# Performance work log

Measured on AMD Instinct MI355X. Metric: run time of the kernel, lower is better.

The kernel has to match this reference:

```python
import jax, jax.numpy as jnp
import numpy as np

N_NODES = 50000
N_EDGES = 800000
D_IN = 128
D_HID = 128
D_OUT = 2


def setup_inputs() -> dict:
    key = jax.random.key(0)
    ks = jax.random.split(key, 8)
    x = jax.random.normal(ks[0], (N_NODES, D_IN), dtype=jnp.float32)
    edge_index = jax.random.randint(ks[1], (2, N_EDGES), 0, N_NODES, dtype=jnp.int64)
    s = 0.05
    W1_l = jax.random.normal(ks[2], (D_HID, D_IN), dtype=jnp.float32) * s
    W1_r = jax.random.normal(ks[3], (D_HID, D_IN), dtype=jnp.float32) * s
    b1 = jax.random.normal(ks[4], (D_HID,), dtype=jnp.float32) * s
    W2_l = jax.random.normal(ks[5], (D_OUT, D_HID), dtype=jnp.float32) * s
    W2_r = jax.random.normal(ks[6], (D_OUT, D_HID), dtype=jnp.float32) * s
    b2 = jax.random.normal(ks[7], (D_OUT,), dtype=jnp.float32) * s
    return {"x": x, "edge_index": edge_index, "W1_l": W1_l, "W1_r": W1_r,
            "b1": b1, "W2_l": W2_l, "W2_r": W2_r, "b2": b2}


def _sage_conv(x, src, dst, W_l, W_r, b):
    # mean-aggregate neighbor features: gather from src, scatter-sum to dst
    n = x.shape[0]
    msg = x[src]                                            # [E, d]
    agg = jax.ops.segment_sum(msg, dst, num_segments=n)      # [n, d]
    cnt = jax.ops.segment_sum(jnp.ones((src.shape[0],), x.dtype), dst,
                              num_segments=n)
    agg = agg / jnp.maximum(cnt, 1.0)[:, None]
    # lin_l(aggregated) + lin_r(self) + bias  (PyG SAGEConv with root_weight)
    return agg @ W_l.T + x @ W_r.T + b


def reference(x, edge_index, W1_l, W1_r, b1, W2_l, W2_r, b2):
    src, dst = edge_index[0], edge_index[1]
    h = _sage_conv(x, src, dst, W1_l, W1_r, b1)
    h = jax.nn.relu(h)
    out = _sage_conv(h, src, dst, W2_l, W2_r, b2)
    return out
```

## Files before the change

### kernel.cpp

```cpp
#include <hip/hip_runtime.h>

#define N_NODES 50000
#define N_EDGES 800000
#define CAP 48
#define NCHUNK 391

typedef __bf16 bf16_8 __attribute__((ext_vector_type(8)));
typedef float  f32_4  __attribute__((ext_vector_type(4)));
typedef unsigned short u16;
typedef unsigned char  u8;


__device__ __forceinline__ void f8cvt(int2 q, float f[8]) {
    f[0] = __builtin_amdgcn_cvt_f32_fp8(q.x, 0);
    f[1] = __builtin_amdgcn_cvt_f32_fp8(q.x, 1);
    f[2] = __builtin_amdgcn_cvt_f32_fp8(q.x, 2);
    f[3] = __builtin_amdgcn_cvt_f32_fp8(q.x, 3);
    f[4] = __builtin_amdgcn_cvt_f32_fp8(q.y, 0);
    f[5] = __builtin_amdgcn_cvt_f32_fp8(q.y, 1);
    f[6] = __builtin_amdgcn_cvt_f32_fp8(q.y, 2);
    f[7] = __builtin_amdgcn_cvt_f32_fp8(q.y, 3);
}

__global__ void prep_kernel(const float* __restrict__ W1l, const float* __restrict__ W1r,
                            __bf16* __restrict__ Wt, const float* __restrict__ x,
                            u8* __restrict__ xb8,
                            const int* __restrict__ src, const int* __restrict__ dst,
                            int* __restrict__ deg_p, u16* __restrict__ bins) {
    int b = blockIdx.x;
    if (b < 8 * NCHUNK) {
        const int chunk = b >> 3;
        const unsigned cls = b & 7;
        const int base = chunk * 2048;
        int t = base + (int)cls * 256 + threadIdx.x;
        if (t < 16 * N_NODES) {
            int node = t >> 4, c8 = t & 15;
            const f32_4* xp = (const f32_4*)(x + node * 128 + c8 * 8);
            f32_4 v0 = __builtin_nontemporal_load(xp);
            f32_4 v1 = __builtin_nontemporal_load(xp + 1);
            int lo = __builtin_amdgcn_cvt_pk_fp8_f32(v0[0], v0[1], 0, false);
            lo     = __builtin_amdgcn_cvt_pk_fp8_f32(v0[2], v0[3], lo, true);
            int hi = __builtin_amdgcn_cvt_pk_fp8_f32(v1[0], v1[1], 0, false);
            hi     = __builtin_amdgcn_cvt_pk_fp8_f32(v1[2], v1[3], hi, true);
            *(int2*)(xb8 + t * 8) = make_int2(lo, hi);
        }
        #pragma unroll
        for (int k = 0; k < 8; ++k) {
            int e = base + k * 256 + threadIdx.x;
            if (e < N_EDGES) {
                int d = dst[e];
                if (__umulhi((unsigned)d, 687195u) == cls) {
                    int s = src[e];
                    int pos = atomicAdd(&deg_p[d * 16], 1);
                    if (pos < CAP) bins[d * CAP + pos] = (u16)s;
                }
            }
        }
    } else {
        int t = (b - 8 * NCHUNK) * 256 + threadIdx.x;
        int n = t >> 8, k = t & 255;
        float v = (k < 128) ? W1l[n * 128 + k] : W1r[n * 128 + (k - 128)];
        Wt[t] = (__bf16)v;
    }
}

#define LDA 264
__global__ __launch_bounds__(256) void gather_gemm_kernel(
    const int* __restrict__ deg_p, const u16* __restrict__ bins,
    const float* __restrict__ x, const u8* __restrict__ xb8,
    const __bf16* __restrict__ Wt,
    const float* __restrict__ b1, const float* __restrict__ W2l,
    const float* __restrict__ W2r, float* __restrict__ y, float* __restrict__ z)
{
    __shared__ __bf16 As[16 * LDA];
    __shared__ float4 sp[4][16];

    const int i0 = blockIdx.x * 16;
    const int tid = threadIdx.x;
    const int row = tid >> 4, c8 = tid & 15;
    const int gi = i0 + row;

    {
        const f32_4* sxp = (const f32_4*)(x + gi * 128 + c8 * 8);
        f32_4 v0 = __builtin_nontemporal_load(sxp);
        f32_4 v1 = __builtin_nontemporal_load(sxp + 1);
        bf16_8 sv;
        sv[0] = (__bf16)v0[0]; sv[1] = (__bf16)v0[1]; sv[2] = (__bf16)v0[2]; sv[3] = (__bf16)v0[3];
        sv[4] = (__bf16)v1[0]; sv[5] = (__bf16)v1[1]; sv[6] = (__bf16)v1[2]; sv[7] = (__bf16)v1[3];
        *(bf16_8*)(&As[row * LDA + 128 + c8 * 8]) = sv;
    }

    {
        const u16* bp = bins + gi * CAP;
        int n = min(deg_p[gi * 16], CAP);
        float acc[8] = {};
        int j = 0;
        for (; j + 8 <= n; j += 8) {
            uint4 bq = *(const uint4*)(bp + j);
            int2 q0 = *(const int2*)(xb8 + (bq.x & 0xffff) * 128 + c8 * 8);
            int2 q1 = *(const int2*)(xb8 + (bq.x >> 16)    * 128 + c8 * 8);
            int2 q2 = *(const int2*)(xb8 + (bq.y & 0xffff) * 128 + c8 * 8);
            int2 q3 = *(const int2*)(xb8 + (bq.y >> 16)    * 128 + c8 * 8);
            int2 q4 = *(const int2*)(xb8 + (bq.z & 0xffff) * 128 + c8 * 8);
            int2 q5 = *(const int2*)(xb8 + (bq.z >> 16)    * 128 + c8 * 8);
            int2 q6 = *(const int2*)(xb8 + (bq.w & 0xffff) * 128 + c8 * 8);
            int2 q7 = *(const int2*)(xb8 + (bq.w >> 16)    * 128 + c8 * 8);
            float f0[8], f1[8], f2[8], f3[8], f4[8], f5[8], f6[8], f7[8];
            f8cvt(q0, f0); f8cvt(q1, f1); f8cvt(q2, f2); f8cvt(q3, f3);
            f8cvt(q4, f4); f8cvt(q5, f5); f8cvt(q6, f6); f8cvt(q7, f7);
            #pragma unroll
            for (int u = 0; u < 8; ++u)
                acc[u] += ((f0[u] + f1[u]) + (f2[u] + f3[u])) +
                          ((f4[u] + f5[u]) + (f6[u] + f7[u]));
        }
        if (j + 4 <= n) {
            uint2 bq = *(const uint2*)(bp + j);
            int2 q0 = *(const int2*)(xb8 + (bq.x & 0xffff) * 128 + c8 * 8);
            int2 q1 = *(const int2*)(xb8 + (bq.x >> 16)    * 128 + c8 * 8);
            int2 q2 = *(const int2*)(xb8 + (bq.y & 0xffff) * 128 + c8 * 8);
            int2 q3 = *(const int2*)(xb8 + (bq.y >> 16)    * 128 + c8 * 8);
            float f0[8], f1[8], f2[8], f3[8];
            f8cvt(q0, f0); f8cvt(q1, f1); f8cvt(q2, f2); f8cvt(q3, f3);
            #pragma unroll
            for (int u = 0; u < 8; ++u)
                acc[u] += (f0[u] + f1[u]) + (f2[u] + f3[u]);
            j += 4;
        }
        if (j + 2 <= n) {
            int i0e = bp[j], i1e = bp[j + 1];
            int2 q0 = *(const int2*)(xb8 + i0e * 128 + c8 * 8);
            int2 q1 = *(const int2*)(xb8 + i1e * 128 + c8 * 8);
            float f0[8], f1[8];
            f8cvt(q0, f0); f8cvt(q1, f1);
            #pragma unroll
            for (int u = 0; u < 8; ++u) acc[u] += f0[u] + f1[u];
            j += 2;
        }
        if (j < n) {
            int i0e = bp[j];
            int2 q0 = *(const int2*)(xb8 + i0e * 128 + c8 * 8);
            float f0[8];
            f8cvt(q0, f0);
            #pragma unroll
            for (int u = 0; u < 8; ++u) acc[u] += f0[u];
        }
        float inv = 1.0f / fmaxf((float)n, 1.0f);
        bf16_8 o;
        #pragma unroll
        for (int u = 0; u < 8; ++u) o[u] = (__bf16)(acc[u] * inv);
        *(bf16_8*)(&As[row * LDA + c8 * 8]) = o;
    }
    __syncthreads();

    const int wv = tid >> 6, lane = tid & 63;
    const int mr = lane & 15, q = lane >> 4;
    const int n0 = wv * 2, n1 = wv * 2 + 1;

    f32_4 acc0 = (f32_4){0.f,0.f,0.f,0.f}, acc1 = (f32_4){0.f,0.f,0.f,0.f};
    #pragma unroll
    for (int ks = 0; ks < 8; ++ks) {
        bf16_8 a  = *(const bf16_8*)(&As[mr * LDA + ks * 32 + q * 8]);
        bf16_8 b0 = *(const bf16_8*)(Wt + (n0 * 16 + mr) * 256 + ks * 32 + q * 8);
        bf16_8 bb = *(const bf16_8*)(Wt + (n1 * 16 + mr) * 256 + ks * 32 + q * 8);
        acc0 = __builtin_amdgcn_mfma_f32_16x16x32_bf16(a, b0, acc0, 0, 0, 0);
        acc1 = __builtin_amdgcn_mfma_f32_16x16x32_bf16(a, bb, acc1, 0, 0, 0);
    }

    float py0[4] = {}, py1[4] = {}, pz0[4] = {}, pz1[4] = {};
    #pragma unroll
    for (int ntl = 0; ntl < 2; ++ntl) {
        int col = (wv * 2 + ntl) * 16 + mr;
        f32_4 a = ntl ? acc1 : acc0;
        float bb  = b1[col];
        float wl0 = W2l[col], wl1 = W2l[128 + col];
        float wr0 = W2r[col], wr1 = W2r[128 + col];
        #pragma unroll
        for (int r = 0; r < 4; ++r) {
            float hv = fmaxf(a[r] + bb, 0.f);
            py0[r] += hv * wl0; py1[r] += hv * wl1;
            pz0[r] += hv * wr0; pz1[r] += hv * wr1;
        }
    }
    #pragma unroll
    for (int off = 1; off < 16; off <<= 1) {
        #pragma unroll
        for (int r = 0; r < 4; ++r) {
            py0[r] += __shfl_xor(py0[r], off);
            py1[r] += __shfl_xor(py1[r], off);
            pz0[r] += __shfl_xor(pz0[r], off);
            pz1[r] += __shfl_xor(pz1[r], off);
        }
    }
    if (mr < 4) {
        int r = mr;
        sp[wv][q * 4 + r] = make_float4(py0[r], py1[r], pz0[r], pz1[r]);
    }
    __syncthreads();

    if (tid < 16) {
        float4 a0 = sp[0][tid], a1 = sp[1][tid], a2 = sp[2][tid], a3 = sp[3][tid];
        ((float2*)y)[i0 + tid] = make_float2(a0.x + a1.x + a2.x + a3.x,
                                             a0.y + a1.y + a2.y + a3.y);
        ((float2*)z)[i0 + tid] = make_float2(a0.z + a1.z + a2.z + a3.z,
                                             a0.w + a1.w + a2.w + a3.w);
    }
}

__global__ void final_kernel(const int* __restrict__ deg_p, const u16* __restrict__ bins,
                             const float* __restrict__ y, const float* __restrict__ z,
                             const float* __restrict__ b2, float* __restrict__ out) {
    int t = blockIdx.x * 256 + threadIdx.x;
    int node = t >> 4, p = t & 15;
    const u16* bp = bins + node * CAP;
    int n = min(deg_p[node * 16], CAP);
    float a0 = 0.f, a1 = 0.f;
    for (int j = p; j < n; j += 16) {
        float2 v = ((const float2*)y)[bp[j]];
        a0 += v.x; a1 += v.y;
    }
    a0 += __shfl_xor(a0, 1); a1 += __shfl_xor(a1, 1);
    a0 += __shfl_xor(a0, 2); a1 += __shfl_xor(a1, 2);
    a0 += __shfl_xor(a0, 4); a1 += __shfl_xor(a1, 4);
    a0 += __shfl_xor(a0, 8); a1 += __shfl_xor(a1, 8);
    if (p == 0) {
        float inv = 1.0f / fmaxf((float)n, 1.0f);
        float2 zz = ((const float2*)z)[node];
        ((float2*)out)[node] = make_float2(a0 * inv + zz.x + b2[0],
                                           a1 * inv + zz.y + b2[1]);
    }
}

extern "C" void kernel_launch(void* const* d_in, const int* in_sizes, int n_in,
                              void* d_out, int out_size, void* d_ws, size_t ws_size,
                              hipStream_t stream) {
    const float* x   = (const float*)d_in[0];
    const int*   ei  = (const int*)  d_in[1];
    const float* W1l = (const float*)d_in[2];
    const float* W1r = (const float*)d_in[3];
    const float* b1  = (const float*)d_in[4];
    const float* W2l = (const float*)d_in[5];
    const float* W2r = (const float*)d_in[6];
    const float* b2  = (const float*)d_in[7];
    float* out = (float*)d_out;
    const int* src = ei;
    const int* dst = ei + N_EDGES;

    char* ws = (char*)d_ws;
    int*    deg_p = (int*)   (ws + 0);
    u16*    bins  = (u16*)   (ws + 3200000);
    u8*     xb8   = (u8*)    (ws + 8000000);
    float*  y     = (float*) (ws + 14400000);
    float*  z     = (float*) (ws + 14800000);
    __bf16* Wt    = (__bf16*)(ws + 15200000);

    hipMemsetAsync(deg_p, 0, 3200000, stream);
    prep_kernel<<<8 * NCHUNK + 128, 256, 0, stream>>>(W1l, W1r, Wt, x, xb8, src, dst, deg_p, bins);
    gather_gemm_kernel<<<3125, 256, 0, stream>>>(deg_p, bins, x, xb8, Wt, b1, W2l, W2r, y, z);
    final_kernel<<<3125, 256, 0, stream>>>(deg_p, bins, y, z, b2, out);
}
```

Measured before the change: 175.3 us.

## Process 32 rows per block with 16-byte fp8 gathers and 2x2 MFMA tiles

The gather-GEMM kernel now covers 32 nodes per block instead of 16. Each thread handles 16 features with int4 fp8 loads instead of 8 features with int2 loads, which halves the number of gather instructions per row. Each wave computes two M-tiles, so every Wt B-fragment load feeds twice as many MFMAs. The costs are fewer blocks, bounds checks for the partial last block, and higher register pressure from the 16-wide accumulators.

New measurement: 189.7 us. 1.08x slower.

```diff
diff --git a/kernel.cpp b/kernel.cpp
--- a/kernel.cpp
+++ b/kernel.cpp
@@ -4,6 +4,7 @@
 #define N_EDGES 800000
 #define CAP 48
 #define NCHUNK 391
+#define ROWS 32
 
 typedef __bf16 bf16_8 __attribute__((ext_vector_type(8)));
 typedef float  f32_4  __attribute__((ext_vector_type(4)));
@@ -11,15 +12,23 @@
 typedef unsigned char  u8;
 
 
-__device__ __forceinline__ void f8cvt(int2 q, float f[8]) {
-    f[0] = __builtin_amdgcn_cvt_f32_fp8(q.x, 0);
-    f[1] = __builtin_amdgcn_cvt_f32_fp8(q.x, 1);
-    f[2] = __builtin_amdgcn_cvt_f32_fp8(q.x, 2);
-    f[3] = __builtin_amdgcn_cvt_f32_fp8(q.x, 3);
-    f[4] = __builtin_amdgcn_cvt_f32_fp8(q.y, 0);
-    f[5] = __builtin_amdgcn_cvt_f32_fp8(q.y, 1);
-    f[6] = __builtin_amdgcn_cvt_f32_fp8(q.y, 2);
-    f[7] = __builtin_amdgcn_cvt_f32_fp8(q.y, 3);
+__device__ __forceinline__ void f8cvt16(int4 q, float f[16]) {
+    f[0]  = __builtin_amdgcn_cvt_f32_fp8(q.x, 0);
+    f[1]  = __builtin_amdgcn_cvt_f32_fp8(q.x, 1);
+    f[2]  = __builtin_amdgcn_cvt_f32_fp8(q.x, 2);
+    f[3]  = __builtin_amdgcn_cvt_f32_fp8(q.x, 3);
+    f[4]  = __builtin_amdgcn_cvt_f32_fp8(q.y, 0);
+    f[5]  = __builtin_amdgcn_cvt_f32_fp8(q.y, 1);
+    f[6]  = __builtin_amdgcn_cvt_f32_fp8(q.y, 2);
+    f[7]  = __builtin_amdgcn_cvt_f32_fp8(q.y, 3);
+    f[8]  = __builtin_amdgcn_cvt_f32_fp8(q.z, 0);
+    f[9]  = __builtin_amdgcn_cvt_f32_fp8(q.z, 1);
+    f[10] = __builtin_amdgcn_cvt_f32_fp8(q.z, 2);
+    f[11] = __builtin_amdgcn_cvt_f32_fp8(q.z, 3);
+    f[12] = __builtin_amdgcn_cvt_f32_fp8(q.w, 0);
+    f[13] = __builtin_amdgcn_cvt_f32_fp8(q.w, 1);
+    f[14] = __builtin_amdgcn_cvt_f32_fp8(q.w, 2);
+    f[15] = __builtin_amdgcn_cvt_f32_fp8(q.w, 3);
 }
 
 __global__ void prep_kernel(const float* __restrict__ W1l, const float* __restrict__ W1r,
@@ -72,83 +81,78 @@
     const float* __restrict__ b1, const float* __restrict__ W2l,
     const float* __restrict__ W2r, float* __restrict__ y, float* __restrict__ z)
 {
-    __shared__ __bf16 As[16 * LDA];
-    __shared__ float4 sp[4][16];
-
-    const int i0 = blockIdx.x * 16;
+    __shared__ __bf16 As[ROWS * LDA];
+    __shared__ float4 sp[4][ROWS];
+
+    const int i0 = blockIdx.x * ROWS;
     const int tid = threadIdx.x;
-    const int row = tid >> 4, c8 = tid & 15;
+    const int row = tid >> 3, c4 = tid & 7;
     const int gi = i0 + row;
+    const bool valid = gi < N_NODES;
 
     {
-        const f32_4* sxp = (const f32_4*)(x + gi * 128 + c8 * 8);
-        f32_4 v0 = __builtin_nontemporal_load(sxp);
-        f32_4 v1 = __builtin_nontemporal_load(sxp + 1);
-        bf16_8 sv;
-        sv[0] = (__bf16)v0[0]; sv[1] = (__bf16)v0[1]; sv[2] = (__bf16)v0[2]; sv[3] = (__bf16)v0[3];
-        sv[4] = (__bf16)v1[0]; sv[5] = (__bf16)v1[1]; sv[6] = (__bf16)v1[2]; sv[7] = (__bf16)v1[3];
-        *(bf16_8*)(&As[row * LDA + 128 + c8 * 8]) = sv;
+        bf16_8 a = {}, b = {};
+        if (valid) {
+            const f32_4* sxp = (const f32_4*)(x + gi * 128 + c4 * 16);
+            f32_4 v0 = __builtin_nontemporal_load(sxp);
+            f32_4 v1 = __builtin_nontemporal_load(sxp + 1);
+            f32_4 v2 = __builtin_nontemporal_load(sxp + 2);
+            f32_4 v3 = __builtin_nontemporal_load(sxp + 3);
+            a[0] = (__bf16)v0[0]; a[1] = (__bf16)v0[1]; a[2] = (__bf16)v0[2]; a[3] = (__bf16)v0[3];
+            a[4] = (__bf16)v1[0]; a[5] = (__bf16)v1[1]; a[6] = (__bf16)v1[2]; a[7] = (__bf16)v1[3];
+            b[0] = (__bf16)v2[0]; b[1] = (__bf16)v2[1]; b[2] = (__bf16)v2[2]; b[3] = (__bf16)v2[3];
+            b[4] = (__bf16)v3[0]; b[5] = (__bf16)v3[1]; b[6] = (__bf16)v3[2]; b[7] = (__bf16)v3[3];
+        }
+        *(bf16_8*)(&As[row * LDA + 128 + c4 * 16]) = a;
+        *(bf16_8*)(&As[row * LDA + 128 + c4 * 16 + 8]) = b;
     }
 
     {
-        const u16* bp = bins + gi * CAP;
-        int n = min(deg_p[gi * 16], CAP);
-        float acc[8] = {};
-        int j = 0;
-        for (; j + 8 <= n; j += 8) {
-            uint4 bq = *(const uint4*)(bp + j);
-            int2 q0 = *(const int2*)(xb8 + (bq.x & 0xffff) * 128 + c8 * 8);
-            int2 q1 = *(const int2*)(xb8 + (bq.x >> 16)    * 128 + c8 * 8);
-            int2 q2 = *(const int2*)(xb8 + (bq.y & 0xffff) * 128 + c8 * 8);
-            int2 q3 = *(const int2*)(xb8 + (bq.y >> 16)    * 128 + c8 * 8);
-            int2 q4 = *(const int2*)(xb8 + (bq.z & 0xffff) * 128 + c8 * 8);
-            int2 q5 = *(const int2*)(xb8 + (bq.z >> 16)    * 128 + c8 * 8);
-            int2 q6 = *(const int2*)(xb8 + (bq.w & 0xffff) * 128 + c8 * 8);
-            int2 q7 = *(const int2*)(xb8 + (bq.w >> 16)    * 128 + c8 * 8);
-            float f0[8], f1[8], f2[8], f3[8], f4[8], f5[8], f6[8], f7[8];
-            f8cvt(q0, f0); f8cvt(q1, f1); f8cvt(q2, f2); f8cvt(q3, f3);
-            f8cvt(q4, f4); f8cvt(q5, f5); f8cvt(q6, f6); f8cvt(q7, f7);
-            #pragma unroll
-            for (int u = 0; u < 8; ++u)
-                acc[u] += ((f0[u] + f1[u]) + (f2[u] + f3[u])) +
-                          ((f4[u] + f5[u]) + (f6[u] + f7[u]));
-        }
-        if (j + 4 <= n) {
-            uint2 bq = *(const uint2*)(bp + j);
-            int2 q0 = *(const int2*)(xb8 + (bq.x & 0xffff) * 128 + c8 * 8);
-            int2 q1 = *(const int2*)(xb8 + (bq.x >> 16)    * 128 + c8 * 8);
-            int2 q2 = *(const int2*)(xb8 + (bq.y & 0xffff) * 128 + c8 * 8);
-            int2 q3 = *(const int2*)(xb8 + (bq.y >> 16)    * 128 + c8 * 8);
-            float f0[8], f1[8], f2[8], f3[8];
-            f8cvt(q0, f0); f8cvt(q1, f1); f8cvt(q2, f2); f8cvt(q3, f3);
-            #pragma unroll
-            for (int u = 0; u < 8; ++u)
-                acc[u] += (f0[u] + f1[u]) + (f2[u] + f3[u]);
-            j += 4;
-        }
-        if (j + 2 <= n) {
-            int i0e = bp[j], i1e = bp[j + 1];
-            int2 q0 = *(const int2*)(xb8 + i0e * 128 + c8 * 8);
-            int2 q1 = *(const int2*)(xb8 + i1e * 128 + c8 * 8);
-            float f0[8], f1[8];
-            f8cvt(q0, f0); f8cvt(q1, f1);
-            #pragma unroll
-            for (int u = 0; u < 8; ++u) acc[u] += f0[u] + f1[u];
-            j += 2;
-        }
-        if (j < n) {
-            int i0e = bp[j];
-            int2 q0 = *(const int2*)(xb8 + i0e * 128 + c8 * 8);
-            float f0[8];
-            f8cvt(q0, f0);
-            #pragma unroll
-            for (int u = 0; u < 8; ++u) acc[u] += f0[u];
+        int n = 0;
+        float acc[16] = {};
+        if (valid) {
+            const u16* bp = bins + gi * CAP;
+            n = min(deg_p[gi * 16], CAP);
+            int j = 0;
+            for (; j + 4 <= n; j += 4) {
+                uint2 bq = *(const uint2*)(bp + j);
+                int4 q0 = *(const int4*)(xb8 + (bq.x & 0xffff) * 128 + c4 * 16);
+                int4 q1 = *(const int4*)(xb8 + (bq.x >> 16)    * 128 + c4 * 16);
+                int4 q2 = *(const int4*)(xb8 + (bq.y & 0xffff) * 128 + c4 * 16);
+                int4 q3 = *(const int4*)(xb8 + (bq.y >> 16)    * 128 + c4 * 16);
+                float f0[16], f1[16], f2[16], f3[16];
+                f8cvt16(q0, f0); f8cvt16(q1, f1); f8cvt16(q2, f2); f8cvt16(q3, f3);
+                #pragma unroll
+                for (int u = 0; u < 16; ++u)
+                    acc[u] += (f0[u] + f1[u]) + (f2[u] + f3[u]);
+            }
+            if (j + 2 <= n) {
+                int i0e = bp[j], i1e = bp[j + 1];
+                int4 q0 = *(const int4*)(xb8 + i0e * 128 + c4 * 16);
+                int4 q1 = *(const int4*)(xb8 + i1e * 128 + c4 * 16);
+                float f0[16], f1[16];
+                f8cvt16(q0, f0); f8cvt16(q1, f1);
+                #pragma unroll
+                for (int u = 0; u < 16; ++u) acc[u] += f0[u] + f1[u];
+                j += 2;
+            }
+            if (j < n) {
+                int4 q0 = *(const int4*)(xb8 + bp[j] * 128 + c4 * 16);
+                float f0[16];
+                f8cvt16(q0, f0);
+                #pragma unroll
+                for (int u = 0; u < 16; ++u) acc[u] += f0[u];
+            }
         }
         float inv = 1.0f / fmaxf((float)n, 1.0f);
-        bf16_8 o;
-        #pragma unroll
-        for (int u = 0; u < 8; ++u) o[u] = (__bf16)(acc[u] * inv);
-        *(bf16_8*)(&As[row * LDA + c8 * 8]) = o;
+        bf16_8 o0, o1;
+        #pragma unroll
+        for (int u = 0; u < 8; ++u) {
+            o0[u] = (__bf16)(acc[u] * inv);
+            o1[u] = (__bf16)(acc[u + 8] * inv);
+        }
+        *(bf16_8*)(&As[row * LDA + c4 * 16]) = o0;
+        *(bf16_8*)(&As[row * LDA + c4 * 16 + 8]) = o1;
     }
     __syncthreads();
 
@@ -156,48 +160,62 @@
     const int mr = lane & 15, q = lane >> 4;
     const int n0 = wv * 2, n1 = wv * 2 + 1;
 
-    f32_4 acc0 = (f32_4){0.f,0.f,0.f,0.f}, acc1 = (f32_4){0.f,0.f,0.f,0.f};
+    f32_4 acc00 = (f32_4){0.f,0.f,0.f,0.f}, acc01 = (f32_4){0.f,0.f,0.f,0.f};
+    f32_4 acc10 = (f32_4){0.f,0.f,0.f,0.f}, acc11 = (f32_4){0.f,0.f,0.f,0.f};
     #pragma unroll
     for (int ks = 0; ks < 8; ++ks) {
-        bf16_8 a  = *(const bf16_8*)(&As[mr * LDA + ks * 32 + q * 8]);
+        bf16_8 a0 = *(const bf16_8*)(&As[mr * LDA + ks * 32 + q * 8]);
+        bf16_8 a1 = *(const bf16_8*)(&As[(16 + mr) * LDA + ks * 32 + q * 8]);
         bf16_8 b0 = *(const bf16_8*)(Wt + (n0 * 16 + mr) * 256 + ks * 32 + q * 8);
-        bf16_8 bb = *(const bf16_8*)(Wt + (n1 * 16 + mr) * 256 + ks * 32 + q * 8);
-        acc0 = __builtin_amdgcn_mfma_f32_16x16x32_bf16(a, b0, acc0, 0, 0, 0);
-        acc1 = __builtin_amdgcn_mfma_f32_16x16x32_bf16(a, bb, acc1, 0, 0, 0);
-    }
-
-    float py0[4] = {}, py1[4] = {}, pz0[4] = {}, pz1[4] = {};
+        bf16_8 b1 = *(const bf16_8*)(Wt + (n1 * 16 + mr) * 256 + ks * 32 + q * 8);
+        acc00 = __builtin_amdgcn_mfma_f32_16x16x32_bf16(a0, b0, acc00, 0, 0, 0);
+        acc01 = __builtin_amdgcn_mfma_f32_16x16x32_bf16(a0, b1, acc01, 0, 0, 0);
+        acc10 = __builtin_amdgcn_mfma_f32_16x16x32_bf16(a1, b0, acc10, 0, 0, 0);
+        acc11 = __builtin_amdgcn_mfma_f32_16x16x32_bf16(a1, b1, acc11, 0, 0, 0);
+    }
+
+    float py0[2][4] = {}, py1[2][4] = {}, pz0[2][4] = {}, pz1[2][4] = {};
     #pragma unroll
-    for (int ntl = 0; ntl < 2; ++ntl) {
-        int col = (wv * 2 + ntl) * 16 + mr;
-        f32_4 a = ntl ? acc1 : acc0;
-        float bb  = b1[col];
-        float wl0 = W2l[col], wl1 = W2l[128 + col];
-        float wr0 = W2r[col], wr1 = W2r[128 + col];
-        #pragma unroll
-        for (int r = 0; r < 4; ++r) {
-            float hv = fmaxf(a[r] + bb, 0.f);
-            py0[r] += hv * wl0; py1[r] += hv * wl1;
-            pz0[r] += hv * wr0; pz1[r] += hv * wr1;
+    for (int mh = 0; mh < 2; ++mh) {
+        #pragma unroll
+        for (int ntl = 0; ntl < 2; ++ntl) {
+            int col = (wv * 2 + ntl) * 16 + mr;
+            f32_4 a = (mh == 0) ? (ntl == 0 ? acc00 : acc01)
+                                : (ntl == 0 ? acc10 : acc11);
+            float bb  = b1[col];
+            float wl0 = W2l[col], wl1 = W2l[128 + col];
+            float wr0 = W2r[col], wr1 = W2r[128 + col];
+            #pragma unroll
+            for (int r = 0; r < 4; ++r) {
+                float hv = fmaxf(a[r] + bb, 0.f);
+                py0[mh][r] += hv * wl0; py1[mh][r] += hv * wl1;
+                pz0[mh][r] += hv * wr0; pz1[mh][r] += hv * wr1;
+            }
         }
     }
     #pragma unroll
     for (int off = 1; off < 16; off <<= 1) {
         #pragma unroll
-        for (int r = 0; r < 4; ++r) {
-            py0[r] += __shfl_xor(py0[r], off);
-            py1[r] += __shfl_xor(py1[r], off);
-            pz0[r] += __shfl_xor(pz0[r], off);
-            pz1[r] += __shfl_xor(pz1[r], off);
+        for (int mh = 0; mh < 2; ++mh) {
+            #pragma unroll
+            for (int r = 0; r < 4; ++r) {
+                py0[mh][r] += __shfl_xor(py0[mh][r], off);
+                py1[mh][r] += __shfl_xor(py1[mh][r], off);
+                pz0[mh][r] += __shfl_xor(pz0[mh][r], off);
+                pz1[mh][r] += __shfl_xor(pz1[mh][r], off);
+            }
         }
     }
     if (mr < 4) {
         int r = mr;
-        sp[wv][q * 4 + r] = make_float4(py0[r], py1[r], pz0[r], pz1[r]);
+        #pragma unroll
+        for (int mh = 0; mh < 2; ++mh)
+            sp[wv][mh * 16 + q * 4 + r] =
+                make_float4(py0[mh][r], py1[mh][r], pz0[mh][r], pz1[mh][r]);
     }
     __syncthreads();
 
-    if (tid < 16) {
+    if (tid < ROWS && i0 + tid < N_NODES) {
         float4 a0 = sp[0][tid], a1 = sp[1][tid], a2 = sp[2][tid], a3 = sp[3][tid];
         ((float2*)y)[i0 + tid] = make_float2(a0.x + a1.x + a2.x + a3.x,
                                              a0.y + a1.y + a2.y + a3.y);
@@ -255,6 +273,6 @@
 
     hipMemsetAsync(deg_p, 0, 3200000, stream);
     prep_kernel<<<8 * NCHUNK + 128, 256, 0, stream>>>(W1l, W1r, Wt, x, xb8, src, dst, deg_p, bins);
-    gather_gemm_kernel<<<3125, 256, 0, stream>>>(deg_p, bins, x, xb8, Wt, b1, W2l, W2r, y, z);
+    gather_gemm_kernel<<<1563, 256, 0, stream>>>(deg_p, bins, x, xb8, Wt, b1, W2l, W2r, y, z);
     final_kernel<<<3125, 256, 0, stream>>>(deg_p, bins, y, z, b2, out);
 }
```
